# Optimization experiments

Measured on AMD Instinct MI355X. Metric: run time of the kernel, lower is better.

The kernel has to match this reference:

```python
import jax, jax.numpy as jnp
import numpy as np

N, E, D, H, C = 50000, 1600000, 128, 2, 32

def setup_inputs() -> dict:
    key = jax.random.key(0)
    ks = jax.random.split(key, 8)
    x = jax.random.normal(ks[0], (N, D), jnp.float32)
    edge_index = jax.random.randint(ks[1], (2, E), 0, N)
    intra_enrichment_weights = jax.random.uniform(ks[2], (E,), jnp.float32)
    W = jax.random.normal(ks[3], (D, H * C), jnp.float32) * (1.0 / np.sqrt(D))
    att_src = jax.random.normal(ks[4], (H, C), jnp.float32) * 0.1
    att_dst = jax.random.normal(ks[5], (H, C), jnp.float32) * 0.1
    bias = jnp.zeros((H * C,), jnp.float32)
    enrichment_scale = jnp.asarray(0.01, jnp.float32)
    return dict(x=x, edge_index=edge_index,
                intra_enrichment_weights=intra_enrichment_weights,
                W=W, att_src=att_src, att_dst=att_dst, bias=bias,
                enrichment_scale=enrichment_scale)

def reference(x, edge_index, intra_enrichment_weights, W, att_src, att_dst, bias, enrichment_scale):
    n = x.shape[0]
    xf = jax.nn.elu(x)                       # F.elu on input features
    h = (xf @ W).reshape(n, H, C)            # [N, heads, out]
    # GATConv default add_self_loops=True
    loop = jnp.arange(n, dtype=edge_index.dtype)
    src = jnp.concatenate([edge_index[0], loop])
    dst = jnp.concatenate([edge_index[1], loop])
    a_src = jnp.einsum('nhc,hc->nh', h, att_src)   # [N, H]
    a_dst = jnp.einsum('nhc,hc->nh', h, att_dst)
    alpha = jax.nn.leaky_relu(a_src[src] + a_dst[dst], 0.2)  # [E+N, H]
    # softmax over incoming edges per destination node
    m = jax.ops.segment_max(alpha, dst, num_segments=n)
    e = jnp.exp(alpha - m[dst])
    denom = jax.ops.segment_sum(e, dst, num_segments=n)
    p = e / denom[dst]                       # every node has a self-loop -> denom > 0
    out = jax.ops.segment_sum(h[src] * p[:, :, None], dst, num_segments=n)  # [N, H, C]
    out = out.reshape(n, H * C) + bias
    # enrichment bias (scatter-mean of per-edge weights over source nodes)
    s0 = edge_index[0]
    nw = jax.ops.segment_sum(intra_enrichment_weights, s0, num_segments=n)
    cnt = jax.ops.segment_sum(jnp.ones_like(intra_enrichment_weights), s0, num_segments=n)
    nw = nw / jnp.maximum(cnt, 1.0)
    nw = jnp.clip(nw, 0.2, 5.0)
    scale_factor = 0.1 * jax.nn.sigmoid(enrichment_scale)
    return out + scale_factor * (nw[:, None] - 1.0)
```

## Files before the change

### kernel.cpp

```cpp
#include <hip/hip_runtime.h>


typedef unsigned int u32;
typedef unsigned short u16;

#define SLOTS2 2624
#define NB2_MAX 800
#define EPB 4096

#define XS 136
#define CS 68

#define SMEM_F 34816

typedef __attribute__((ext_vector_type(8))) short short8;
typedef __attribute__((ext_vector_type(4))) float float4v;

__device__ __forceinline__ u16 f2bf(float f) {
    union { float f; u32 u; } v; v.f = f;
    u32 r = v.u + 0x7fffu + ((v.u >> 16) & 1u);
    return (u16)(r >> 16);
}
__device__ __forceinline__ float bf2f(u16 u) {
    union { u32 i; float f; } v; v.i = ((u32)u) << 16; return v.f;
}
__device__ __forceinline__ float bf_lo(u32 u) {
    union { u32 i; float f; } v; v.i = u << 16; return v.f;
}
__device__ __forceinline__ float bf_hi(u32 u) {
    union { u32 i; float f; } v; v.i = u & 0xFFFF0000u; return v.f;
}
__device__ __forceinline__ void bf_split(float v, short& hi, short& lo) {
    u16 h = f2bf(v);
    float hf = bf2f(h);
    hi = (short)h;
    lo = (short)f2bf(v - hf);
}

__global__ void k_prep(const float* __restrict__ Wm,
                       short* __restrict__ Whf, short* __restrict__ Wlf,
                       int* cursA, int* cursB)
{
    int t = threadIdx.x;
    for (int i = t; i < NB2_MAX; i += 256) { cursA[i] = 0; cursB[i] = 0; }
    for (int p = t; p < 1024; p += 256) {
        int frag = p >> 6, l = p & 63;
        int ks = frag >> 2, nt = frag & 3;
        int q = l >> 4, m = l & 15;
        int f = nt * 16 + m;
#pragma unroll
        for (int j = 0; j < 8; ++j) {
            int k = ks * 32 + q * 8 + j;
            float wv = Wm[k * 64 + f];
            short hi, lo; bf_split(wv, hi, lo);
            Whf[p * 8 + j] = hi;
            Wlf[p * 8 + j] = lo;
        }
    }
}

static __device__ __forceinline__ void node_body(
    char* smem, int nb_id,
    const float* __restrict__ x,
    const short* __restrict__ Whf, const short* __restrict__ Wlf,
    const float* __restrict__ att_s, const float* __restrict__ att_d,
    u32* __restrict__ hb32, float* __restrict__ a_src, float* __restrict__ a_dst,
    int nN)
{
    short* Ah = (short*)smem;
    short* Al = (short*)(smem + 17408);
    float* Cl = (float*)Ah;

    int t = threadIdx.x;
    int n0 = nb_id * 64;

    for (int j = 0; j < 8; ++j) {
        int idx = t + 256 * j;
        int r = idx >> 5, c4 = idx & 31;
        int gn = n0 + r;
        float4 xv = make_float4(0.f, 0.f, 0.f, 0.f);
        if (gn < nN) xv = ((const float4*)x)[(size_t)gn * 32 + c4];
        float e[4];
        e[0] = xv.x > 0.f ? xv.x : __expf(xv.x) - 1.f;
        e[1] = xv.y > 0.f ? xv.y : __expf(xv.y) - 1.f;
        e[2] = xv.z > 0.f ? xv.z : __expf(xv.z) - 1.f;
        e[3] = xv.w > 0.f ? xv.w : __expf(xv.w) - 1.f;
        short h4[4], l4[4];
#pragma unroll
        for (int i = 0; i < 4; ++i) bf_split(e[i], h4[i], l4[i]);
        *(short4*)&Ah[r * XS + c4 * 4] = make_short4(h4[0], h4[1], h4[2], h4[3]);
        *(short4*)&Al[r * XS + c4 * 4] = make_short4(l4[0], l4[1], l4[2], l4[3]);
    }
    __syncthreads();

    {
        int w = t >> 6, l = t & 63;
        int q = l >> 4, m = l & 15;
        int arow = w * 16 + m;
        float4v acc[4] = {};
#pragma unroll
        for (int ks = 0; ks < 4; ++ks) {
            int k0 = ks * 32 + q * 8;
            short8 ah = *(const short8*)&Ah[arow * XS + k0];
            short8 al = *(const short8*)&Al[arow * XS + k0];
#pragma unroll
            for (int nt = 0; nt < 4; ++nt) {
                short8 bh = *(const short8*)&Whf[((ks * 4 + nt) * 64 + l) * 8];
                short8 bl = *(const short8*)&Wlf[((ks * 4 + nt) * 64 + l) * 8];
                acc[nt] = __builtin_amdgcn_mfma_f32_16x16x32_bf16(ah, bh, acc[nt], 0, 0, 0);
                acc[nt] = __builtin_amdgcn_mfma_f32_16x16x32_bf16(ah, bl, acc[nt], 0, 0, 0);
                acc[nt] = __builtin_amdgcn_mfma_f32_16x16x32_bf16(al, bh, acc[nt], 0, 0, 0);
            }
        }
        __syncthreads();
#pragma unroll
        for (int nt = 0; nt < 4; ++nt)
#pragma unroll
            for (int r = 0; r < 4; ++r)
                Cl[(w * 16 + q * 4 + r) * CS + nt * 16 + m] = acc[nt][r];
    }
    __syncthreads();

    {
        int nl = t >> 2, fq = t & 3;
        int gn = n0 + nl;
        float ps = 0.f, pd = 0.f;
        if (gn < nN) {
            float hv[16];
#pragma unroll
            for (int i = 0; i < 16; ++i) {
                int f = fq * 16 + i;
                hv[i] = Cl[nl * CS + f];
                ps = fmaf(hv[i], att_s[f], ps);
                pd = fmaf(hv[i], att_d[f], pd);
            }
#pragma unroll
            for (int i = 0; i < 8; ++i) {
                u32 pk = ((u32)f2bf(hv[2 * i + 1]) << 16) | (u32)f2bf(hv[2 * i]);
                hb32[(size_t)gn * 32 + fq * 8 + i] = pk;
            }
        }
        float ps2 = ps + __shfl_xor(ps, 1, 64);
        float pd2 = pd + __shfl_xor(pd, 1, 64);
        if (gn < nN && (fq & 1) == 0) {
            a_src[2 * gn + (fq >> 1)] = ps2;
            a_dst[2 * gn + (fq >> 1)] = pd2;
        }
    }
}

static __device__ __forceinline__ void partA_body(
    char* smem, int pa_id,
    const int* __restrict__ ei, const float* __restrict__ wgt,
    int* cursA, int* cursB, u32* bufA, u32* bufB, int E, int nb2)
{
    u32* arr  = (u32*)smem;
    int* cnt  = (int*)(smem + 16384);
    int* lofs = (int*)(smem + 19584);
    int* bas  = (int*)(smem + 22784);
    int* part = (int*)(smem + 25984);

    int t = threadIdx.x;
    int base = pa_id * EPB;
    int nv = min(EPB, E - base);
    int sv[16], dv[16]; float wv[16];
#pragma unroll
    for (int k = 0; k < 16; ++k) {
        int e = base + k * 256 + t;
        if (e < E) { sv[k] = ei[e]; dv[k] = ei[E + e]; wv[k] = wgt[e]; }
        else       { sv[k] = -1;    dv[k] = -1;        wv[k] = 0.f; }
    }

#pragma unroll
    for (int side = 0; side < 2; ++side) {
        int* curs = side ? cursB : cursA;
        u32* buf  = side ? bufB  : bufA;

        for (int b = t; b < nb2; b += 256) cnt[b] = 0;
        __syncthreads();
#pragma unroll
        for (int k = 0; k < 16; ++k) {
            int key = side ? sv[k] : dv[k];
            if (key >= 0) atomicAdd(&cnt[key >> 6], 1);
        }
        __syncthreads();
        for (int b = t; b < nb2; b += 256) {
            int c = cnt[b];
            if (c > 0) bas[b] = atomicAdd(&curs[b], c);
        }
        __syncthreads();
        {
            int c[4]; int s = 0;
#pragma unroll
            for (int i = 0; i < 4; ++i) {
                int bb = 4 * t + i;
                c[i] = (bb < nb2) ? cnt[bb] : 0;
                s += c[i];
            }
            part[t] = s;
            __syncthreads();
            for (int off = 1; off < 256; off <<= 1) {
                int v = (t >= off) ? part[t - off] : 0;
                __syncthreads();
                part[t] += v;
                __syncthreads();
            }
            int excl = part[t] - s;
#pragma unroll
            for (int i = 0; i < 4; ++i) {
                int bb = 4 * t + i;
                if (bb < nb2) lofs[bb] = excl;
                excl += c[i];
            }
        }
        __syncthreads();
        for (int b = t; b < nb2; b += 256) cnt[b] = 0;
        __syncthreads();
#pragma unroll
        for (int k = 0; k < 16; ++k) {
            int key = side ? sv[k] : dv[k];
            if (key >= 0) {
                int bk = key >> 6;
                int r = lofs[bk] + atomicAdd(&cnt[bk], 1);
                u32 payload;
                if (side) {
                    u32 wq = (u32)(wv[k] * 65536.f);
                    if (wq > 0xFFFFu) wq = 0xFFFFu;
                    payload = ((u32)(key & 63) << 16) | wq;
                } else {
                    payload = ((u32)(key & 63) << 16) | (u32)sv[k];
                }
                arr[r] = ((u32)bk << 22) | payload;
            }
        }
        __syncthreads();
        for (int i = t; i < nv; i += 256) {
            u32 va = arr[i];
            int bk = va >> 22;
            int g = bas[bk] + (i - lofs[bk]);
            if (g < SLOTS2) buf[(size_t)bk * SLOTS2 + g] = va & 0x3FFFFFu;
        }
        __syncthreads();
    }
}

__global__ __launch_bounds__(256) void k_fused(
    const float* __restrict__ x,
    const short* __restrict__ Whf, const short* __restrict__ Wlf,
    const float* __restrict__ att_s, const float* __restrict__ att_d,
    u32* __restrict__ hb32, float* __restrict__ a_src, float* __restrict__ a_dst,
    const int* __restrict__ ei, const float* __restrict__ wgt,
    int* cursA, int* cursB, u32* bufA, u32* bufB,
    int E, int nb2, int nblkA, int nN)
{
    __shared__ __align__(16) char smem[SMEM_F];
    int bid = blockIdx.x;
    int q3 = bid / 3;
    if ((bid % 3) == 0 && q3 < nblkA) {
        partA_body(smem, q3, ei, wgt, cursA, cursB, bufA, bufB, E, nb2);
    } else {
        int npa_before = min(q3 + ((bid % 3) ? 1 : 0), nblkA);
        node_body(smem, bid - npa_before, x, Whf, Wlf, att_s, att_d,
                  hb32, a_src, a_dst, nN);
    }
}

__global__ __launch_bounds__(512) void k_final(
    const u32* __restrict__ hb32,
    const float* __restrict__ a_src, const float* __restrict__ a_dst,
    const u32* __restrict__ bufA, const int* __restrict__ cursA,
    const u32* __restrict__ bufB, const int* __restrict__ cursB,
    const float* __restrict__ bias, const float* __restrict__ esc,
    float* __restrict__ out, int nN)
{
    __shared__ u32 st[SLOTS2];
    __shared__ u16 st2[SLOTS2];
    __shared__ int ldeg[64], lscan[64], lcur[64];
    __shared__ int usum[64], ucnt[64];

    int b = blockIdx.x, t = threadIdx.x;
    int n0 = b << 6;
    int nA = cursA[b]; if (nA > SLOTS2) nA = SLOTS2;
    int nB = cursB[b]; if (nB > SLOTS2) nB = SLOTS2;

    if (t < 64) { ldeg[t] = 0; lcur[t] = 0; usum[t] = 0; ucnt[t] = 0; }
    __syncthreads();
    for (int i = t; i < nA; i += 512) {
        u32 v = bufA[(size_t)b * SLOTS2 + i];
        st[i] = v;
        atomicAdd(&ldeg[v >> 16], 1);
    }
    for (int i = t; i < nB; i += 512) {
        u32 v = bufB[(size_t)b * SLOTS2 + i];
        atomicAdd(&usum[v >> 16], (int)(v & 0xFFFFu));
        atomicAdd(&ucnt[v >> 16], 1);
    }
    __syncthreads();
    if (t < 64) lscan[t] = ldeg[t];
    __syncthreads();
    for (int off = 1; off < 64; off <<= 1) {
        int v = 0;
        if (t < 64 && t >= off) v = lscan[t - off];
        __syncthreads();
        if (t < 64) lscan[t] += v;
        __syncthreads();
    }
    if (t < 64) lscan[t] -= ldeg[t];
    __syncthreads();
    for (int i = t; i < nA; i += 512) {
        u32 v = st[i];
        int dl = v >> 16;
        int pos = lscan[dl] + atomicAdd(&lcur[dl], 1);
        st2[pos] = (u16)(v & 0xFFFFu);
    }
    __syncthreads();

    int ws = t >> 6, lane = t & 63;
    int q = lane >> 4, fl = lane & 15, head = fl >> 3;
    const uint2* hb2 = (const uint2*)hb32;
    float escv = esc[0];
    float sf = 0.1f / (1.f + __expf(-escv));
    float4 bb = ((const float4*)bias)[fl];

    for (int dl0 = ws; dl0 < 64; dl0 += 16) {
        int dlA = dl0, dlB = dl0 + 8;
        int gnA = n0 + dlA, gnB = n0 + dlB;
        if (gnA >= nN) break;
        bool vB = (gnB < nN);

        int begA = lscan[dlA], cntA = ldeg[dlA];
        float2 advA = ((const float2*)a_dst)[gnA];
        float2 asvA = ((const float2*)a_src)[gnA];
        float tA0 = asvA.x + advA.x; tA0 = tA0 > 0.f ? tA0 : 0.2f * tA0;
        float tA1 = asvA.y + advA.y; tA1 = tA1 > 0.f ? tA1 : 0.2f * tA1;
        float esA0 = __expf(tA0), esA1 = __expf(tA1);
        float aA0 = 0.f, aA1 = 0.f, aA2 = 0.f, aA3 = 0.f;
        if (q == 0) {
            float eself = head ? esA1 : esA0;
            uint2 hs = hb2[(size_t)gnA * 16 + fl];
            aA0 = eself * bf_lo(hs.x); aA1 = eself * bf_hi(hs.x);
            aA2 = eself * bf_lo(hs.y); aA3 = eself * bf_hi(hs.y);
        }
        float dsA = 0.f;

        int begB = 0, cntB = 0;
        float2 advB = make_float2(0.f, 0.f);
        float esB0 = 0.f, esB1 = 0.f;
        float aB0 = 0.f, aB1 = 0.f, aB2 = 0.f, aB3 = 0.f;
        float dsB = 0.f;
        if (vB) {
            begB = lscan[dlB]; cntB = ldeg[dlB];
            advB = ((const float2*)a_dst)[gnB];
            float2 asvB = ((const float2*)a_src)[gnB];
            float tB0 = asvB.x + advB.x; tB0 = tB0 > 0.f ? tB0 : 0.2f * tB0;
            float tB1 = asvB.y + advB.y; tB1 = tB1 > 0.f ? tB1 : 0.2f * tB1;
            esB0 = __expf(tB0); esB1 = __expf(tB1);
            if (q == 0) {
                float eself = head ? esB1 : esB0;
                uint2 hs = hb2[(size_t)gnB * 16 + fl];
                aB0 = eself * bf_lo(hs.x); aB1 = eself * bf_hi(hs.x);
                aB2 = eself * bf_lo(hs.y); aB3 = eself * bf_hi(hs.y);
            }
        }

        int nwA = (cntA + 63) >> 6, nwB = (cntB + 63) >> 6;
        int nwin = nwA > nwB ? nwA : nwB;
        for (int w = 0; w < nwin; ++w) {
            int b0 = w << 6;
            u32 siA = (u32)gnA; float eA0 = 0.f, eA1 = 0.f; int wnA = 0;
            if (w < nwA) {
                wnA = cntA - b0; if (wnA > 64) wnA = 64;
                if (lane < wnA) {
                    siA = (u32)st2[begA + b0 + lane];
                    float2 ap = ((const float2*)a_src)[siA];
                    float v0 = ap.x + advA.x; v0 = v0 > 0.f ? v0 : 0.2f * v0;
                    float v1 = ap.y + advA.y; v1 = v1 > 0.f ? v1 : 0.2f * v1;
                    eA0 = __expf(v0); eA1 = __expf(v1);
                }
            }
            u32 siB = (u32)gnA; float eB0 = 0.f, eB1 = 0.f; int wnB = 0;
            if (w < nwB) {
                wnB = cntB - b0; if (wnB > 64) wnB = 64;
                if (lane < wnB) {
                    siB = (u32)st2[begB + b0 + lane];
                    float2 ap = ((const float2*)a_src)[siB];
                    float v0 = ap.x + advB.x; v0 = v0 > 0.f ? v0 : 0.2f * v0;
                    float v1 = ap.y + advB.y; v1 = v1 > 0.f ? v1 : 0.2f * v1;
                    eB0 = __expf(v0); eB1 = __expf(v1);
                }
            }
            int wmax = wnA > wnB ? wnA : wnB;
            int iters = (wmax + 3) >> 2;
#pragma unroll 4
            for (int k = 0; k < iters; ++k) {
                int e = 4 * k + q;
                u32 rsiA = __shfl(siA, e, 64);
                u32 rsiB = __shfl(siB, e, 64);
                uint2 hvA = hb2[(size_t)rsiA * 16 + fl];
                uint2 hvB = hb2[(size_t)rsiB * 16 + fl];
                float w0A = __shfl(eA0, e, 64), w1A = __shfl(eA1, e, 64);
                float w0B = __shfl(eB0, e, 64), w1B = __shfl(eB1, e, 64);
                float wA = head ? w1A : w0A;
                float wB = head ? w1B : w0B;
                dsA += wA; dsB += wB;
                aA0 = fmaf(wA, bf_lo(hvA.x), aA0);
                aA1 = fmaf(wA, bf_hi(hvA.x), aA1);
                aA2 = fmaf(wA, bf_lo(hvA.y), aA2);
                aA3 = fmaf(wA, bf_hi(hvA.y), aA3);
                aB0 = fmaf(wB, bf_lo(hvB.x), aB0);
                aB1 = fmaf(wB, bf_hi(hvB.x), aB1);
                aB2 = fmaf(wB, bf_lo(hvB.y), aB2);
                aB3 = fmaf(wB, bf_hi(hvB.y), aB3);
            }
        }
        dsA += __shfl_xor(dsA, 16, 64); dsA += __shfl_xor(dsA, 32, 64);
        dsB += __shfl_xor(dsB, 16, 64); dsB += __shfl_xor(dsB, 32, 64);
        aA0 += __shfl_xor(aA0, 16, 64); aA0 += __shfl_xor(aA0, 32, 64);
        aA1 += __shfl_xor(aA1, 16, 64); aA1 += __shfl_xor(aA1, 32, 64);
        aA2 += __shfl_xor(aA2, 16, 64); aA2 += __shfl_xor(aA2, 32, 64);
        aA3 += __shfl_xor(aA3, 16, 64); aA3 += __shfl_xor(aA3, 32, 64);
        aB0 += __shfl_xor(aB0, 16, 64); aB0 += __shfl_xor(aB0, 32, 64);
        aB1 += __shfl_xor(aB1, 16, 64); aB1 += __shfl_xor(aB1, 32, 64);
        aB2 += __shfl_xor(aB2, 16, 64); aB2 += __shfl_xor(aB2, 32, 64);
        aB3 += __shfl_xor(aB3, 16, 64); aB3 += __shfl_xor(aB3, 32, 64);

        if (q == 0) {
            {
                float den = (head ? esA1 : esA0) + dsA;
                float inv = 1.f / den;
                float cntf = (float)ucnt[dlA];
                float nw = ((float)usum[dlA] * (1.f / 65536.f)) / fmaxf(cntf, 1.f);
                nw = fminf(fmaxf(nw, 0.2f), 5.f);
                float en = sf * (nw - 1.f);
                float4 o;
                o.x = aA0 * inv + bb.x + en;
                o.y = aA1 * inv + bb.y + en;
                o.z = aA2 * inv + bb.z + en;
                o.w = aA3 * inv + bb.w + en;
                ((float4*)out)[(size_t)gnA * 16 + fl] = o;
            }
            if (vB) {
                float den = (head ? esB1 : esB0) + dsB;
                float inv = 1.f / den;
                float cntf = (float)ucnt[dlB];
                float nw = ((float)usum[dlB] * (1.f / 65536.f)) / fmaxf(cntf, 1.f);
                nw = fminf(fmaxf(nw, 0.2f), 5.f);
                float en = sf * (nw - 1.f);
                float4 o;
                o.x = aB0 * inv + bb.x + en;
                o.y = aB1 * inv + bb.y + en;
                o.z = aB2 * inv + bb.z + en;
                o.w = aB3 * inv + bb.w + en;
                ((float4*)out)[(size_t)gnB * 16 + fl] = o;
            }
        }
    }
}

extern "C" void kernel_launch(void* const* d_in, const int* in_sizes, int n_in,
                              void* d_out, int out_size, void* d_ws, size_t ws_size,
                              hipStream_t stream)
{
    const float* x     = (const float*)d_in[0];
    const int*   ei    = (const int*)d_in[1];
    const float* wgt   = (const float*)d_in[2];
    const float* Wm    = (const float*)d_in[3];
    const float* att_s = (const float*)d_in[4];
    const float* att_d = (const float*)d_in[5];
    const float* bias  = (const float*)d_in[6];
    const float* esc   = (const float*)d_in[7];
    float* out = (float*)d_out;

    int nN = in_sizes[0] / 128;
    int E  = in_sizes[2];
    int NB2 = (nN + 63) / 64;

    char* p = (char*)d_ws;
    auto alloc = [&](size_t bytes) -> char* {
        char* r = p; p += (bytes + 255) & ~(size_t)255; return r;
    };
    u32*   hb32  = (u32*)  alloc((size_t)nN * 32 * 4);
    float* a_src = (float*)alloc((size_t)nN * 2 * 4);
    float* a_dst = (float*)alloc((size_t)nN * 2 * 4);
    short* Whf   = (short*)alloc(16 * 64 * 8 * 2);
    short* Wlf   = (short*)alloc(16 * 64 * 8 * 2);
    int*   cursA = (int*)  alloc(NB2_MAX * 4);
    int*   cursB = (int*)  alloc(NB2_MAX * 4);
    u32*   bufA  = (u32*)  alloc((size_t)NB2 * SLOTS2 * 4);
    u32*   bufB  = (u32*)  alloc((size_t)NB2 * SLOTS2 * 4);

    int nblkA = (E + EPB - 1) / EPB;
    int nblkN = (nN + 63) / 64;
    int nblkF = nblkA + nblkN;

    k_prep<<<dim3(1), dim3(256), 0, stream>>>(Wm, Whf, Wlf, cursA, cursB);
    k_fused<<<dim3(nblkF), dim3(256), 0, stream>>>(x, Whf, Wlf, att_s, att_d,
                                                   hb32, a_src, a_dst,
                                                   ei, wgt, cursA, cursB, bufA, bufB,
                                                   E, NB2, nblkA, nN);
    k_final<<<dim3(NB2), dim3(512), 0, stream>>>(hb32, a_src, a_dst, bufA, cursA,
                                                 bufB, cursB, bias, esc, out, nN);
}
```

Measured before the change: 177.8 us.

## Split edge bucket-sort into separate dst and src blocks interleaved with node blocks

Each edge chunk's two bucketing passes (by destination for attention, by source for enrichment weights) now run in two separate blocks instead of one block doing both serially. The fused kernel's block interleaving changes from a 1-in-3 to a 2-in-4 pattern, and the grid gains one more set of sort blocks. This doubles the parallelism of the sort phase and shortens the per-block critical path, at the cost of reading the edge index chunk in two blocks and launching more blocks.

```diff
diff --git a/kernel.cpp b/kernel.cpp
--- a/kernel.cpp
+++ b/kernel.cpp
@@ -149,10 +149,10 @@
     }
 }
 
-static __device__ __forceinline__ void partA_body(
-    char* smem, int pa_id,
+static __device__ __forceinline__ void sort_body(
+    char* smem, int pa_id, int sideB,
     const int* __restrict__ ei, const float* __restrict__ wgt,
-    int* cursA, int* cursB, u32* bufA, u32* bufB, int E, int nb2)
+    int* curs, u32* buf, int E, int nb2)
 {
     u32* arr  = (u32*)smem;
     int* cnt  = (int*)(smem + 16384);
@@ -163,84 +163,75 @@
     int t = threadIdx.x;
     int base = pa_id * EPB;
     int nv = min(EPB, E - base);
-    int sv[16], dv[16]; float wv[16];
+    int key[16]; u32 pay[16];
 #pragma unroll
     for (int k = 0; k < 16; ++k) {
         int e = base + k * 256 + t;
-        if (e < E) { sv[k] = ei[e]; dv[k] = ei[E + e]; wv[k] = wgt[e]; }
-        else       { sv[k] = -1;    dv[k] = -1;        wv[k] = 0.f; }
-    }
-
-#pragma unroll
-    for (int side = 0; side < 2; ++side) {
-        int* curs = side ? cursB : cursA;
-        u32* buf  = side ? bufB  : bufA;
-
-        for (int b = t; b < nb2; b += 256) cnt[b] = 0;
+        if (e < E) {
+            if (sideB) {
+                key[k] = ei[e];
+                u32 wq = (u32)(wgt[e] * 65536.f);
+                if (wq > 0xFFFFu) wq = 0xFFFFu;
+                pay[k] = wq;
+            } else {
+                key[k] = ei[E + e];
+                pay[k] = (u32)ei[e];
+            }
+        } else { key[k] = -1; pay[k] = 0u; }
+    }
+
+    for (int b = t; b < nb2; b += 256) cnt[b] = 0;
+    __syncthreads();
+#pragma unroll
+    for (int k = 0; k < 16; ++k)
+        if (key[k] >= 0) atomicAdd(&cnt[key[k] >> 6], 1);
+    __syncthreads();
+    for (int b = t; b < nb2; b += 256) {
+        int c = cnt[b];
+        if (c > 0) bas[b] = atomicAdd(&curs[b], c);
+    }
+    __syncthreads();
+    {
+        int c[4]; int s = 0;
+#pragma unroll
+        for (int i = 0; i < 4; ++i) {
+            int bb = 4 * t + i;
+            c[i] = (bb < nb2) ? cnt[bb] : 0;
+            s += c[i];
+        }
+        part[t] = s;
         __syncthreads();
-#pragma unroll
-        for (int k = 0; k < 16; ++k) {
-            int key = side ? sv[k] : dv[k];
-            if (key >= 0) atomicAdd(&cnt[key >> 6], 1);
-        }
-        __syncthreads();
-        for (int b = t; b < nb2; b += 256) {
-            int c = cnt[b];
-            if (c > 0) bas[b] = atomicAdd(&curs[b], c);
-        }
-        __syncthreads();
-        {
-            int c[4]; int s = 0;
-#pragma unroll
-            for (int i = 0; i < 4; ++i) {
-                int bb = 4 * t + i;
-                c[i] = (bb < nb2) ? cnt[bb] : 0;
-                s += c[i];
-            }
-            part[t] = s;
+        for (int off = 1; off < 256; off <<= 1) {
+            int v = (t >= off) ? part[t - off] : 0;
             __syncthreads();
-            for (int off = 1; off < 256; off <<= 1) {
-                int v = (t >= off) ? part[t - off] : 0;
-                __syncthreads();
-                part[t] += v;
-                __syncthreads();
-            }
-            int excl = part[t] - s;
-#pragma unroll
-            for (int i = 0; i < 4; ++i) {
-                int bb = 4 * t + i;
-                if (bb < nb2) lofs[bb] = excl;
-                excl += c[i];
-            }
-        }
-        __syncthreads();
-        for (int b = t; b < nb2; b += 256) cnt[b] = 0;
-        __syncthreads();
-#pragma unroll
-        for (int k = 0; k < 16; ++k) {
-            int key = side ? sv[k] : dv[k];
-            if (key >= 0) {
-                int bk = key >> 6;
-                int r = lofs[bk] + atomicAdd(&cnt[bk], 1);
-                u32 payload;
-                if (side) {
-                    u32 wq = (u32)(wv[k] * 65536.f);
-                    if (wq > 0xFFFFu) wq = 0xFFFFu;
-                    payload = ((u32)(key & 63) << 16) | wq;
-                } else {
-                    payload = ((u32)(key & 63) << 16) | (u32)sv[k];
-                }
-                arr[r] = ((u32)bk << 22) | payload;
-            }
-        }
-        __syncthreads();
-        for (int i = t; i < nv; i += 256) {
-            u32 va = arr[i];
-            int bk = va >> 22;
-            int g = bas[bk] + (i - lofs[bk]);
-            if (g < SLOTS2) buf[(size_t)bk * SLOTS2 + g] = va & 0x3FFFFFu;
-        }
-        __syncthreads();
+            part[t] += v;
+            __syncthreads();
+        }
+        int excl = part[t] - s;
+#pragma unroll
+        for (int i = 0; i < 4; ++i) {
+            int bb = 4 * t + i;
+            if (bb < nb2) lofs[bb] = excl;
+            excl += c[i];
+        }
+    }
+    __syncthreads();
+    for (int b = t; b < nb2; b += 256) cnt[b] = 0;
+    __syncthreads();
+#pragma unroll
+    for (int k = 0; k < 16; ++k) {
+        if (key[k] >= 0) {
+            int bk = key[k] >> 6;
+            int r = lofs[bk] + atomicAdd(&cnt[bk], 1);
+            arr[r] = ((u32)bk << 22) | ((u32)(key[k] & 63) << 16) | pay[k];
+        }
+    }
+    __syncthreads();
+    for (int i = t; i < nv; i += 256) {
+        u32 va = arr[i];
+        int bk = va >> 22;
+        int g = bas[bk] + (i - lofs[bk]);
+        if (g < SLOTS2) buf[(size_t)bk * SLOTS2 + g] = va & 0x3FFFFFu;
     }
 }
 
@@ -255,12 +246,15 @@
 {
     __shared__ __align__(16) char smem[SMEM_F];
     int bid = blockIdx.x;
-    int q3 = bid / 3;
-    if ((bid % 3) == 0 && q3 < nblkA) {
-        partA_body(smem, q3, ei, wgt, cursA, cursB, bufA, bufB, E, nb2);
+    int g = bid >> 2, r = bid & 3;
+    if (g < nblkA && r == 0) {
+        sort_body(smem, g, 0, ei, wgt, cursA, bufA, E, nb2);
+    } else if (g < nblkA && r == 2) {
+        sort_body(smem, g, 1, ei, wgt, cursB, bufB, E, nb2);
     } else {
-        int npa_before = min(q3 + ((bid % 3) ? 1 : 0), nblkA);
-        node_body(smem, bid - npa_before, x, Whf, Wlf, att_s, att_d,
+        int sortBefore = (g < nblkA) ? (2 * g + (r >= 1 ? 1 : 0) + (r >= 3 ? 1 : 0))
+                                     : 2 * nblkA;
+        node_body(smem, bid - sortBefore, x, Whf, Wlf, att_s, att_d,
                   hb32, a_src, a_dst, nN);
     }
 }
@@ -491,7 +485,7 @@
 
     int nblkA = (E + EPB - 1) / EPB;
     int nblkN = (nN + 63) / 64;
-    int nblkF = nblkA + nblkN;
+    int nblkF = 2 * nblkA + nblkN;
 
     k_prep<<<dim3(1), dim3(256), 0, stream>>>(Wm, Whf, Wlf, cursA, cursB);
     k_fused<<<dim3(nblkF), dim3(256), 0, stream>>>(x, Whf, Wlf, att_s, att_d,
```

Result: faster. 170.4 us (median of 2 runs) (-4.1%).
